# Performance work log

Measured on AMD Instinct MI355X. Metric: run time of the kernel, lower is better.

Reference implementation:

```python
import jax, jax.numpy as jnp
import numpy as np

B, N, D = 4096, 64, 128

def setup_inputs() -> dict:
    key = jax.random.key(0)
    ks = jax.random.split(key, 5)
    return {
        "stu_emb": jax.random.normal(ks[0], (B, D), jnp.float32),
        "concept_emb": jax.random.normal(ks[1], (B, D), jnp.float32),
        "neighbor_emb": jax.random.normal(ks[2], (B, N, D), jnp.float32),
        # Linear(2D -> D) for stu_concept_integration (xavier-like scale)
        "Ws": jax.random.normal(ks[3], (2 * D, D), jnp.float32) * (2.0 / (3 * D)) ** 0.5,
        "bs": jnp.full((D,), 0.1, jnp.float32),
        # Linear(2D -> 1) for concept_neighbor_weight
        "Ww": jax.random.normal(ks[4], (2 * D, 1), jnp.float32) * (2.0 / (2 * D + 1)) ** 0.5,
        "bw": jnp.full((1,), 0.1, jnp.float32),
    }


def reference(stu_emb, concept_emb, neighbor_emb, Ws, bs, Ww, bw):
    # Masks: 1 where the (first) concatenated input is nonzero along features
    dt = stu_emb.dtype
    mask_s = (jnp.sum(stu_emb, -1, keepdims=True) != 0).astype(dt)[:, None, :]      # [B,1,1]
    mask_c = (jnp.sum(concept_emb, -1, keepdims=True) != 0).astype(dt)[:, None, :]  # [B,1,1]

    # Split concat-linear into two halves so the broadcasted half is computed once
    Ws_a, Ws_b = Ws[:D], Ws[D:]   # [D,D] each
    Ww_a, Ww_b = Ww[:D], Ww[D:]   # [D,1] each

    stu_part = stu_emb @ Ws_a            # [B,D]
    con_part = concept_emb @ Ws_b        # [B,D]
    nbr_part = neighbor_emb @ Ws_b       # [B,N,D]

    # neighbor attention weights: Linear(2D->1)(cat(concept_ext, neighbor)) * mask_c
    w = (concept_emb @ Ww_a)[:, None, :] + neighbor_emb @ Ww_b + bw  # [B,N,1]
    w = w * mask_c
    w = jax.nn.softmax(w, axis=-2)  # softmax over neighbor axis

    # stu integrated with neighbors / with the original concept, masked by stu mask
    integ_n = (stu_part[:, None, :] + nbr_part + bs) * mask_s            # [B,N,D]
    integ_o = (stu_part[:, None, :] + con_part[:, None, :] + bs) * mask_s  # [B,N,D] (broadcast)

    # combine over neighbor axis and average the two branches
    y = jnp.sum(integ_o + w * integ_n, axis=-2) / 2  # [B,D]
    return y
```

## Files before the change

### kernel.cpp

```cpp
#include <hip/hip_runtime.h>

#define BB 4096
#define NN 64
#define DD 128
#define G  4
#define P2S 36

#define LDS_BARRIER() asm volatile("s_waitcnt lgkmcnt(0)\n\ts_barrier" ::: "memory")

__global__ __launch_bounds__(256) void kFused(
    const float* __restrict__ stu,
    const float* __restrict__ conc,
    const float* __restrict__ nbr,
    const float* __restrict__ Ws,
    const float* __restrict__ bs,
    const float* __restrict__ Ww,
    float* __restrict__ y)
{
    const int t    = threadIdx.x;
    const int q    = t & 63;
    const int cg   = t & 31;
    const int g8   = t >> 5;
    const int wv   = t >> 6;
    const int b0   = blockIdx.x * G;

    __shared__ __align__(16) float part2[NN * P2S];
    __shared__ float dsum[2][4];
    __shared__ float csum[G];
    __shared__ float maskh[G];
    __shared__ __align__(16) float u[G][2 * DD];
    __shared__ __align__(16) float scratch[G * 8 * DD];

    const float4 wb = reinterpret_cast<const float4*>(Ww + DD)[cg];
    const float4* nb4 = reinterpret_cast<const float4*>(nbr);
    const float4* Ws4 = reinterpret_cast<const float4*>(Ws);

    {
        const int b = b0 + wv;
        float cv0 = conc[(size_t)b * DD + q];
        float cv1 = conc[(size_t)b * DD + 64 + q];
        float sv0 = stu [(size_t)b * DD + q];
        float sv1 = stu [(size_t)b * DD + 64 + q];
        u[wv][q]           = 65.0f * sv0;
        u[wv][64 + q]      = 65.0f * sv1;
        u[wv][DD + q]      = 64.0f * cv0;
        u[wv][DD + 64 + q] = 64.0f * cv1;
        float cs = cv0 + cv1, ss = sv0 + sv1;
#pragma unroll
        for (int o = 1; o < 64; o <<= 1) {
            cs += __shfl_xor(cs, o);
            ss += __shfl_xor(ss, o);
        }
        if (q == 0) {
            csum[wv]  = cs;
            maskh[wv] = (ss != 0.0f) ? 0.5f : 0.0f;
        }
    }

    float4 valA[8], valB[8];
#pragma unroll
    for (int i = 0; i < 8; ++i)
        valA[i] = nb4[(size_t)b0 * 2048 + t + 256 * i];

    const int rown  = 2 * wv + (q & 1) + 8 * ((q >> 1) & 7);
    const int chunk = ((q >> 4) + ((q >> 1) & 7)) & 3;
    const int srcb  = (g8 & 1);

#pragma unroll
    for (int g = 0; g < G; ++g) {
        float4* valc = (g & 1) ? valB : valA;
        float4* valp = (g & 1) ? valA : valB;

#pragma unroll
        for (int i = 0; i < 8; ++i) {
            const int row = g8 + 8 * i;
            part2[row * P2S + cg] =
                valc[i].x * wb.x + valc[i].y * wb.y + valc[i].z * wb.z + valc[i].w * wb.w;
        }
        if (g < G - 1) {
#pragma unroll
            for (int i = 0; i < 8; ++i)
                valp[i] = nb4[(size_t)(b0 + g + 1) * 2048 + t + 256 * i];
        }

        float s;
        {
            const float4 pa = *reinterpret_cast<const float4*>(&part2[rown * P2S + chunk * 8]);
            const float4 pb = *reinterpret_cast<const float4*>(&part2[rown * P2S + chunk * 8 + 4]);
            s = pa.x + pa.y + pa.z + pa.w + pb.x + pb.y + pb.z + pb.w;
            s += __shfl_xor(s, 16);
            s += __shfl_xor(s, 32);
        }
        const float e = __expf(s);
        float s16 = e;
        s16 += __shfl_xor(s16, 1);
        s16 += __shfl_xor(s16, 2);
        s16 += __shfl_xor(s16, 4);
        s16 += __shfl_xor(s16, 8);
        if (q == 0) dsum[g & 1][wv] = s16;
        LDS_BARRIER();

        const float den  = dsum[g & 1][0] + dsum[g & 1][1] + dsum[g & 1][2] + dsum[g & 1][3];
        const float rden = 1.0f / den;
        const bool  uni  = (csum[g] == 0.0f);
        float4 a = {0.f, 0.f, 0.f, 0.f};
#pragma unroll
        for (int i = 0; i < 8; ++i) {
            const float we = __shfl(e, srcb + 2 * i);
            const float w  = uni ? 0.015625f : we * rden;
            a.x += w * valc[i].x; a.y += w * valc[i].y;
            a.z += w * valc[i].z; a.w += w * valc[i].w;
        }
        reinterpret_cast<float4*>(scratch + g * 8 * DD)[g8 * 32 + cg] = a;
    }
    __syncthreads();

#pragma unroll
    for (int it = 0; it < 2; ++it) {
        const int idx = t + 256 * it;
        const int gg  = idx >> 7;
        const int c   = idx & 127;
        float s2 = 0.0f;
#pragma unroll
        for (int k = 0; k < 8; ++k) s2 += scratch[gg * 8 * DD + k * DD + c];
        u[gg][DD + c] += s2;
    }
    __syncthreads();

    float4 acc0 = {0,0,0,0}, acc1 = {0,0,0,0}, acc2 = {0,0,0,0}, acc3 = {0,0,0,0};
#pragma unroll 4
    for (int j = 0; j < 32; ++j) {
        const int k = g8 * 32 + j;
        float4 wq = Ws4[k * 32 + cg];
        float u0 = u[0][k], u1 = u[1][k], u2 = u[2][k], u3 = u[3][k];
        acc0.x += u0 * wq.x; acc0.y += u0 * wq.y; acc0.z += u0 * wq.z; acc0.w += u0 * wq.w;
        acc1.x += u1 * wq.x; acc1.y += u1 * wq.y; acc1.z += u1 * wq.z; acc1.w += u1 * wq.w;
        acc2.x += u2 * wq.x; acc2.y += u2 * wq.y; acc2.z += u2 * wq.z; acc2.w += u2 * wq.w;
        acc3.x += u3 * wq.x; acc3.y += u3 * wq.y; acc3.z += u3 * wq.z; acc3.w += u3 * wq.w;
    }
    {
        float4* pr = reinterpret_cast<float4*>(scratch);
        pr[(g8 * G + 0) * 32 + cg] = acc0;
        pr[(g8 * G + 1) * 32 + cg] = acc1;
        pr[(g8 * G + 2) * 32 + cg] = acc2;
        pr[(g8 * G + 3) * 32 + cg] = acc3;
    }
    __syncthreads();
#pragma unroll
    for (int i = 0; i < 2; ++i) {
        const int idx = t + 256 * i;
        const int r = idx >> 7;
        const int c = idx & 127;
        float s2 = 0.0f;
#pragma unroll
        for (int k2 = 0; k2 < 8; ++k2) s2 += scratch[(k2 * G + r) * DD + c];
        y[(size_t)(b0 + r) * DD + c] = (s2 + 65.0f * bs[c]) * maskh[r];
    }
}

extern "C" void kernel_launch(void* const* d_in, const int* in_sizes, int n_in,
                              void* d_out, int out_size, void* d_ws, size_t ws_size,
                              hipStream_t stream) {
    const float* stu  = (const float*)d_in[0];
    const float* conc = (const float*)d_in[1];
    const float* nbr  = (const float*)d_in[2];
    const float* Ws   = (const float*)d_in[3];
    const float* bs   = (const float*)d_in[4];
    const float* Ww   = (const float*)d_in[5];
    float* y = (float*)d_out;

    kFused<<<BB / G, 256, 0, stream>>>(stu, conc, nbr, Ws, bs, Ww, y);
}
```

Baseline: 29.34 us.

## Restructure fused kernel to 8 batches per 512-thread block with shuffle reductions

Doubles the batch rows per block to 8 and the block size to 512 threads. Each thread now holds two full neighbor rows in registers, so the attention logits come from in-wave shuffle reductions instead of an LDS partial-dot table. The weighted neighbor sum is also reduced with shuffles, and its cross-wave reduction is pipelined into the next batch iteration. The Ws GEMV then processes 8 rows with 4 k-groups, which halves the grid and amortizes Ws loads over more rows, at the cost of fewer blocks and more shuffle traffic.

```diff
diff --git a/kernel.cpp b/kernel.cpp
--- a/kernel.cpp
+++ b/kernel.cpp
@@ -3,12 +3,14 @@
 #define BB 4096
 #define NN 64
 #define DD 128
-#define G  4
-#define P2S 36
+#define G  8
+#define VPS 132
 
 #define LDS_BARRIER() asm volatile("s_waitcnt lgkmcnt(0)\n\ts_barrier" ::: "memory")
 
-__global__ __launch_bounds__(256) void kFused(
+#define DOT4(a, b) ((a).x*(b).x + (a).y*(b).y + (a).z*(b).z + (a).w*(b).w)
+
+__global__ __launch_bounds__(512) void kFused(
     const float* __restrict__ stu,
     const float* __restrict__ conc,
     const float* __restrict__ nbr,
@@ -17,34 +19,42 @@
     const float* __restrict__ Ww,
     float* __restrict__ y)
 {
-    const int t    = threadIdx.x;
-    const int q    = t & 63;
-    const int cg   = t & 31;
-    const int g8   = t >> 5;
-    const int wv   = t >> 6;
-    const int b0   = blockIdx.x * G;
+    const int t  = threadIdx.x;
+    const int q  = t & 63;
+    const int w  = t >> 6;
+    const int b0 = blockIdx.x * G;
 
-    __shared__ __align__(16) float part2[NN * P2S];
-    __shared__ float dsum[2][4];
+    __shared__ __align__(16) float scratch[4096];
+    __shared__ __align__(16) float dsum[2][8];
     __shared__ float csum[G];
     __shared__ float maskh[G];
     __shared__ __align__(16) float u[G][2 * DD];
-    __shared__ __align__(16) float scratch[G * 8 * DD];
 
-    const float4 wb = reinterpret_cast<const float4*>(Ww + DD)[cg];
     const float4* nb4 = reinterpret_cast<const float4*>(nbr);
     const float4* Ws4 = reinterpret_cast<const float4*>(Ws);
+    const float4* Ww4 = reinterpret_cast<const float4*>(Ww + DD);
+    const float4 wb0 = Ww4[2 * (q & 15)];
+    const float4 wb1 = Ww4[2 * (q & 15) + 1];
+
+    float4 vA[4], vB[4];
+    {
+        const size_t tb = (size_t)b0 * 2048;
+        vA[0] = nb4[tb + 2 * t];
+        vA[1] = nb4[tb + 2 * t + 1];
+        vA[2] = nb4[tb + 1024 + 2 * t];
+        vA[3] = nb4[tb + 1024 + 2 * t + 1];
+    }
 
     {
-        const int b = b0 + wv;
+        const int b = b0 + w;
         float cv0 = conc[(size_t)b * DD + q];
         float cv1 = conc[(size_t)b * DD + 64 + q];
         float sv0 = stu [(size_t)b * DD + q];
         float sv1 = stu [(size_t)b * DD + 64 + q];
-        u[wv][q]           = 65.0f * sv0;
-        u[wv][64 + q]      = 65.0f * sv1;
-        u[wv][DD + q]      = 64.0f * cv0;
-        u[wv][DD + 64 + q] = 64.0f * cv1;
+        u[w][q]           = 65.0f * sv0;
+        u[w][64 + q]      = 65.0f * sv1;
+        u[w][DD + q]      = 64.0f * cv0;
+        u[w][DD + 64 + q] = 64.0f * cv1;
         float cs = cv0 + cv1, ss = sv0 + sv1;
 #pragma unroll
         for (int o = 1; o < 64; o <<= 1) {
@@ -52,109 +62,114 @@
             ss += __shfl_xor(ss, o);
         }
         if (q == 0) {
-            csum[wv]  = cs;
-            maskh[wv] = (ss != 0.0f) ? 0.5f : 0.0f;
+            csum[w]  = cs;
+            maskh[w] = (ss != 0.0f) ? 0.5f : 0.0f;
         }
     }
 
-    float4 valA[8], valB[8];
-#pragma unroll
-    for (int i = 0; i < 8; ++i)
-        valA[i] = nb4[(size_t)b0 * 2048 + t + 256 * i];
-
-    const int rown  = 2 * wv + (q & 1) + 8 * ((q >> 1) & 7);
-    const int chunk = ((q >> 4) + ((q >> 1) & 7)) & 3;
-    const int srcb  = (g8 & 1);
-
 #pragma unroll
     for (int g = 0; g < G; ++g) {
-        float4* valc = (g & 1) ? valB : valA;
-        float4* valp = (g & 1) ? valA : valB;
+        float4* valc = (g & 1) ? vB : vA;
+        float4* valp = (g & 1) ? vA : vB;
 
+        float p0 = DOT4(valc[0], wb0) + DOT4(valc[1], wb1);
+        float p1 = DOT4(valc[2], wb0) + DOT4(valc[3], wb1);
 #pragma unroll
-        for (int i = 0; i < 8; ++i) {
-            const int row = g8 + 8 * i;
-            part2[row * P2S + cg] =
-                valc[i].x * wb.x + valc[i].y * wb.y + valc[i].z * wb.z + valc[i].w * wb.w;
+        for (int o = 1; o < 16; o <<= 1) {
+            p0 += __shfl_xor(p0, o);
+            p1 += __shfl_xor(p1, o);
         }
+        const float e0 = __expf(p0);
+        const float e1 = __expf(p1);
+        float es = e0 + e1;
+        es += __shfl_xor(es, 16);
+        es += __shfl_xor(es, 32);
+        if (q == 0) dsum[g & 1][w] = es;
+
         if (g < G - 1) {
-#pragma unroll
-            for (int i = 0; i < 8; ++i)
-                valp[i] = nb4[(size_t)(b0 + g + 1) * 2048 + t + 256 * i];
+            const size_t nb = (size_t)(b0 + g + 1) * 2048;
+            valp[0] = nb4[nb + 2 * t];
+            valp[1] = nb4[nb + 2 * t + 1];
+            valp[2] = nb4[nb + 1024 + 2 * t];
+            valp[3] = nb4[nb + 1024 + 2 * t + 1];
         }
-
-        float s;
-        {
-            const float4 pa = *reinterpret_cast<const float4*>(&part2[rown * P2S + chunk * 8]);
-            const float4 pb = *reinterpret_cast<const float4*>(&part2[rown * P2S + chunk * 8 + 4]);
-            s = pa.x + pa.y + pa.z + pa.w + pb.x + pb.y + pb.z + pb.w;
-            s += __shfl_xor(s, 16);
-            s += __shfl_xor(s, 32);
-        }
-        const float e = __expf(s);
-        float s16 = e;
-        s16 += __shfl_xor(s16, 1);
-        s16 += __shfl_xor(s16, 2);
-        s16 += __shfl_xor(s16, 4);
-        s16 += __shfl_xor(s16, 8);
-        if (q == 0) dsum[g & 1][wv] = s16;
         LDS_BARRIER();
 
-        const float den  = dsum[g & 1][0] + dsum[g & 1][1] + dsum[g & 1][2] + dsum[g & 1][3];
+        const float4 d0 = *reinterpret_cast<const float4*>(&dsum[g & 1][0]);
+        const float4 d1 = *reinterpret_cast<const float4*>(&dsum[g & 1][4]);
+        const float den = d0.x + d0.y + d0.z + d0.w + d1.x + d1.y + d1.z + d1.w;
         const float rden = 1.0f / den;
         const bool  uni  = (csum[g] == 0.0f);
-        float4 a = {0.f, 0.f, 0.f, 0.f};
+        const float w0 = uni ? 0.015625f : e0 * rden;
+        const float w1 = uni ? 0.015625f : e1 * rden;
+        float4 a0, a1;
+        a0.x = w0 * valc[0].x + w1 * valc[2].x;
+        a0.y = w0 * valc[0].y + w1 * valc[2].y;
+        a0.z = w0 * valc[0].z + w1 * valc[2].z;
+        a0.w = w0 * valc[0].w + w1 * valc[2].w;
+        a1.x = w0 * valc[1].x + w1 * valc[3].x;
+        a1.y = w0 * valc[1].y + w1 * valc[3].y;
+        a1.z = w0 * valc[1].z + w1 * valc[3].z;
+        a1.w = w0 * valc[1].w + w1 * valc[3].w;
+        a0.x += __shfl_xor(a0.x, 16); a0.x += __shfl_xor(a0.x, 32);
+        a0.y += __shfl_xor(a0.y, 16); a0.y += __shfl_xor(a0.y, 32);
+        a0.z += __shfl_xor(a0.z, 16); a0.z += __shfl_xor(a0.z, 32);
+        a0.w += __shfl_xor(a0.w, 16); a0.w += __shfl_xor(a0.w, 32);
+        a1.x += __shfl_xor(a1.x, 16); a1.x += __shfl_xor(a1.x, 32);
+        a1.y += __shfl_xor(a1.y, 16); a1.y += __shfl_xor(a1.y, 32);
+        a1.z += __shfl_xor(a1.z, 16); a1.z += __shfl_xor(a1.z, 32);
+        a1.w += __shfl_xor(a1.w, 16); a1.w += __shfl_xor(a1.w, 32);
+        if (q < 16) {
+            float* vp = &scratch[(g & 1) * 2048 + w * VPS + q * 8];
+            *reinterpret_cast<float4*>(vp)     = a0;
+            *reinterpret_cast<float4*>(vp + 4) = a1;
+        }
+        if (g > 0 && t < DD) {
+            const float* vp = &scratch[((g - 1) & 1) * 2048];
+            float s = 0.0f;
 #pragma unroll
-        for (int i = 0; i < 8; ++i) {
-            const float we = __shfl(e, srcb + 2 * i);
-            const float w  = uni ? 0.015625f : we * rden;
-            a.x += w * valc[i].x; a.y += w * valc[i].y;
-            a.z += w * valc[i].z; a.w += w * valc[i].w;
+            for (int k = 0; k < 8; ++k) s += vp[k * VPS + t];
+            u[g - 1][DD + t] += s;
         }
-        reinterpret_cast<float4*>(scratch + g * 8 * DD)[g8 * 32 + cg] = a;
+    }
+
+    LDS_BARRIER();
+    if (t < DD) {
+        const float* vp = &scratch[((G - 1) & 1) * 2048];
+        float s = 0.0f;
+#pragma unroll
+        for (int k = 0; k < 8; ++k) s += vp[k * VPS + t];
+        u[G - 1][DD + t] += s;
     }
     __syncthreads();
 
-#pragma unroll
-    for (int it = 0; it < 2; ++it) {
-        const int idx = t + 256 * it;
-        const int gg  = idx >> 7;
-        const int c   = idx & 127;
-        float s2 = 0.0f;
-#pragma unroll
-        for (int k = 0; k < 8; ++k) s2 += scratch[gg * 8 * DD + k * DD + c];
-        u[gg][DD + c] += s2;
-    }
-    __syncthreads();
-
-    float4 acc0 = {0,0,0,0}, acc1 = {0,0,0,0}, acc2 = {0,0,0,0}, acc3 = {0,0,0,0};
+    const int kg = t >> 7;
+    const int cg = t & 31;
+    const int rh = (t >> 5) & 3;
+    float4 acc0 = {0,0,0,0}, acc1 = {0,0,0,0};
 #pragma unroll 4
-    for (int j = 0; j < 32; ++j) {
-        const int k = g8 * 32 + j;
-        float4 wq = Ws4[k * 32 + cg];
-        float u0 = u[0][k], u1 = u[1][k], u2 = u[2][k], u3 = u[3][k];
+    for (int j = 0; j < 64; ++j) {
+        const int k = kg * 64 + j;
+        const float4 wq = Ws4[k * 32 + cg];
+        const float u0 = u[rh * 2][k], u1 = u[rh * 2 + 1][k];
         acc0.x += u0 * wq.x; acc0.y += u0 * wq.y; acc0.z += u0 * wq.z; acc0.w += u0 * wq.w;
         acc1.x += u1 * wq.x; acc1.y += u1 * wq.y; acc1.z += u1 * wq.z; acc1.w += u1 * wq.w;
-        acc2.x += u2 * wq.x; acc2.y += u2 * wq.y; acc2.z += u2 * wq.z; acc2.w += u2 * wq.w;
-        acc3.x += u3 * wq.x; acc3.y += u3 * wq.y; acc3.z += u3 * wq.z; acc3.w += u3 * wq.w;
     }
     {
         float4* pr = reinterpret_cast<float4*>(scratch);
-        pr[(g8 * G + 0) * 32 + cg] = acc0;
-        pr[(g8 * G + 1) * 32 + cg] = acc1;
-        pr[(g8 * G + 2) * 32 + cg] = acc2;
-        pr[(g8 * G + 3) * 32 + cg] = acc3;
+        pr[(kg * 8 + rh * 2    ) * 32 + cg] = acc0;
+        pr[(kg * 8 + rh * 2 + 1) * 32 + cg] = acc1;
     }
     __syncthreads();
 #pragma unroll
     for (int i = 0; i < 2; ++i) {
-        const int idx = t + 256 * i;
+        const int idx = t + 512 * i;
         const int r = idx >> 7;
         const int c = idx & 127;
-        float s2 = 0.0f;
+        float s = 0.0f;
 #pragma unroll
-        for (int k2 = 0; k2 < 8; ++k2) s2 += scratch[(k2 * G + r) * DD + c];
-        y[(size_t)(b0 + r) * DD + c] = (s2 + 65.0f * bs[c]) * maskh[r];
+        for (int k2 = 0; k2 < 4; ++k2) s += scratch[(k2 * 8 + r) * DD + c];
+        y[(size_t)(b0 + r) * DD + c] = (s + 65.0f * bs[c]) * maskh[r];
     }
 }
 
@@ -169,5 +184,5 @@
     const float* Ww   = (const float*)d_in[5];
     float* y = (float*)d_out;
 
-    kFused<<<BB / G, 256, 0, stream>>>(stu, conc, nbr, Ws, bs, Ww, y);
+    kFused<<<BB / G, 512, 0, stream>>>(stu, conc, nbr, Ws, bs, Ww, y);
 }
```

Result: slower. 33.32 us (+13.6%).

## Split fused kernel into per-batch attention pass and batched GEMV pass

Applied to the files above, without the earlier changes.

Replaces the single fused kernel, where each block handled 4 batch rows with a software-pipelined neighbor loop, with two kernels. The first uses one block per batch row to compute the softmax-weighted neighbor sum and writes it to workspace. The second multiplies 8 rows at a time by Ws, which doubles reuse of each Ws load. This gives more parallelism and less serial work per block in the bandwidth-bound first pass, at the cost of a second launch and a round trip of the intermediate through global memory.

```diff
diff --git a/kernel.cpp b/kernel.cpp
--- a/kernel.cpp
+++ b/kernel.cpp
@@ -3,158 +3,160 @@
 #define BB 4096
 #define NN 64
 #define DD 128
-#define G  4
 #define P2S 36
 
 #define LDS_BARRIER() asm volatile("s_waitcnt lgkmcnt(0)\n\ts_barrier" ::: "memory")
+#define DOT4(a, b) ((a).x*(b).x + (a).y*(b).y + (a).z*(b).z + (a).w*(b).w)
 
-__global__ __launch_bounds__(256) void kFused(
-    const float* __restrict__ stu,
+__global__ __launch_bounds__(256) void k1(
     const float* __restrict__ conc,
     const float* __restrict__ nbr,
-    const float* __restrict__ Ws,
-    const float* __restrict__ bs,
     const float* __restrict__ Ww,
-    float* __restrict__ y)
+    float* __restrict__ vout)
 {
-    const int t    = threadIdx.x;
-    const int q    = t & 63;
-    const int cg   = t & 31;
-    const int g8   = t >> 5;
-    const int wv   = t >> 6;
-    const int b0   = blockIdx.x * G;
+    const int t  = threadIdx.x;
+    const int q  = t & 63;
+    const int cg = t & 31;
+    const int g8 = t >> 5;
+    const int wv = t >> 6;
+    const int b  = blockIdx.x;
 
     __shared__ __align__(16) float part2[NN * P2S];
-    __shared__ float dsum[2][4];
-    __shared__ float csum[G];
-    __shared__ float maskh[G];
-    __shared__ __align__(16) float u[G][2 * DD];
-    __shared__ __align__(16) float scratch[G * 8 * DD];
+    __shared__ float dsum[4];
+    __shared__ __align__(16) float scratch[8 * DD];
 
     const float4 wb = reinterpret_cast<const float4*>(Ww + DD)[cg];
-    const float4* nb4 = reinterpret_cast<const float4*>(nbr);
-    const float4* Ws4 = reinterpret_cast<const float4*>(Ws);
+    const float4* nb4 = reinterpret_cast<const float4*>(nbr) + (size_t)b * 2048;
 
-    {
-        const int b = b0 + wv;
-        float cv0 = conc[(size_t)b * DD + q];
-        float cv1 = conc[(size_t)b * DD + 64 + q];
-        float sv0 = stu [(size_t)b * DD + q];
-        float sv1 = stu [(size_t)b * DD + 64 + q];
-        u[wv][q]           = 65.0f * sv0;
-        u[wv][64 + q]      = 65.0f * sv1;
-        u[wv][DD + q]      = 64.0f * cv0;
-        u[wv][DD + 64 + q] = 64.0f * cv1;
-        float cs = cv0 + cv1, ss = sv0 + sv1;
+    float4 val[8];
 #pragma unroll
-        for (int o = 1; o < 64; o <<= 1) {
-            cs += __shfl_xor(cs, o);
-            ss += __shfl_xor(ss, o);
-        }
-        if (q == 0) {
-            csum[wv]  = cs;
-            maskh[wv] = (ss != 0.0f) ? 0.5f : 0.0f;
-        }
-    }
+    for (int i = 0; i < 8; ++i) val[i] = nb4[t + 256 * i];
 
-    float4 valA[8], valB[8];
+    float cs = conc[(size_t)b * DD + q] + conc[(size_t)b * DD + 64 + q];
+#pragma unroll
+    for (int o = 1; o < 64; o <<= 1) cs += __shfl_xor(cs, o);
+
 #pragma unroll
     for (int i = 0; i < 8; ++i)
-        valA[i] = nb4[(size_t)b0 * 2048 + t + 256 * i];
+        part2[(g8 + 8 * i) * P2S + cg] = DOT4(val[i], wb);
 
     const int rown  = 2 * wv + (q & 1) + 8 * ((q >> 1) & 7);
     const int chunk = ((q >> 4) + ((q >> 1) & 7)) & 3;
-    const int srcb  = (g8 & 1);
+    float s;
+    {
+        const float4 pa = *reinterpret_cast<const float4*>(&part2[rown * P2S + chunk * 8]);
+        const float4 pb = *reinterpret_cast<const float4*>(&part2[rown * P2S + chunk * 8 + 4]);
+        s = pa.x + pa.y + pa.z + pa.w + pb.x + pb.y + pb.z + pb.w;
+        s += __shfl_xor(s, 16);
+        s += __shfl_xor(s, 32);
+    }
+    const float e = __expf(s);
+    float s16 = e;
+    s16 += __shfl_xor(s16, 1);
+    s16 += __shfl_xor(s16, 2);
+    s16 += __shfl_xor(s16, 4);
+    s16 += __shfl_xor(s16, 8);
+    if (q == 0) dsum[wv] = s16;
+    LDS_BARRIER();
+
+    const float rden = 1.0f / (dsum[0] + dsum[1] + dsum[2] + dsum[3]);
+    const bool  uni  = (cs == 0.0f);
+    const int   srcb = g8 & 1;
+    float4 a = {0.f, 0.f, 0.f, 0.f};
+#pragma unroll
+    for (int i = 0; i < 8; ++i) {
+        const float we = __shfl(e, srcb + 2 * i);
+        const float w  = uni ? 0.015625f : we * rden;
+        a.x += w * val[i].x; a.y += w * val[i].y;
+        a.z += w * val[i].z; a.w += w * val[i].w;
+    }
+    reinterpret_cast<float4*>(scratch)[g8 * 32 + cg] = a;
+    __syncthreads();
+
+    if (t < 32) {
+        float4 r = {0.f, 0.f, 0.f, 0.f};
+#pragma unroll
+        for (int k = 0; k < 8; ++k) {
+            const float4 p = reinterpret_cast<const float4*>(scratch)[k * 32 + t];
+            r.x += p.x; r.y += p.y; r.z += p.z; r.w += p.w;
+        }
+        reinterpret_cast<float4*>(vout + (size_t)b * DD)[t] = r;
+    }
+}
+
+__global__ __launch_bounds__(256) void k2(
+    const float* __restrict__ stu,
+    const float* __restrict__ conc,
+    const float* vin,
+    const float* __restrict__ Ws,
+    const float* __restrict__ bs,
+    float* y)
+{
+    const int t  = threadIdx.x;
+    const int q  = t & 63;
+    const int wv = t >> 6;
+    const int cg = t & 31;
+    const int b0 = blockIdx.x * 8;
+
+    __shared__ __align__(16) float u[8][2 * DD];
+    __shared__ __align__(16) float pr[8 * 4 * DD];
+    __shared__ float maskh[8];
 
 #pragma unroll
-    for (int g = 0; g < G; ++g) {
-        float4* valc = (g & 1) ? valB : valA;
-        float4* valp = (g & 1) ? valA : valB;
-
+    for (int rr = wv; rr < 8; rr += 4) {
+        const int b = b0 + rr;
+        const float cv0 = conc[(size_t)b * DD + q];
+        const float cv1 = conc[(size_t)b * DD + 64 + q];
+        const float sv0 = stu [(size_t)b * DD + q];
+        const float sv1 = stu [(size_t)b * DD + 64 + q];
+        const float vv0 = vin [(size_t)b * DD + q];
+        const float vv1 = vin [(size_t)b * DD + 64 + q];
+        u[rr][q]           = 65.0f * sv0;
+        u[rr][64 + q]      = 65.0f * sv1;
+        u[rr][DD + q]      = 64.0f * cv0 + vv0;
+        u[rr][DD + 64 + q] = 64.0f * cv1 + vv1;
+        float ss = sv0 + sv1;
 #pragma unroll
-        for (int i = 0; i < 8; ++i) {
-            const int row = g8 + 8 * i;
-            part2[row * P2S + cg] =
-                valc[i].x * wb.x + valc[i].y * wb.y + valc[i].z * wb.z + valc[i].w * wb.w;
-        }
-        if (g < G - 1) {
-#pragma unroll
-            for (int i = 0; i < 8; ++i)
-                valp[i] = nb4[(size_t)(b0 + g + 1) * 2048 + t + 256 * i];
-        }
-
-        float s;
-        {
-            const float4 pa = *reinterpret_cast<const float4*>(&part2[rown * P2S + chunk * 8]);
-            const float4 pb = *reinterpret_cast<const float4*>(&part2[rown * P2S + chunk * 8 + 4]);
-            s = pa.x + pa.y + pa.z + pa.w + pb.x + pb.y + pb.z + pb.w;
-            s += __shfl_xor(s, 16);
-            s += __shfl_xor(s, 32);
-        }
-        const float e = __expf(s);
-        float s16 = e;
-        s16 += __shfl_xor(s16, 1);
-        s16 += __shfl_xor(s16, 2);
-        s16 += __shfl_xor(s16, 4);
-        s16 += __shfl_xor(s16, 8);
-        if (q == 0) dsum[g & 1][wv] = s16;
-        LDS_BARRIER();
-
-        const float den  = dsum[g & 1][0] + dsum[g & 1][1] + dsum[g & 1][2] + dsum[g & 1][3];
-        const float rden = 1.0f / den;
-        const bool  uni  = (csum[g] == 0.0f);
-        float4 a = {0.f, 0.f, 0.f, 0.f};
-#pragma unroll
-        for (int i = 0; i < 8; ++i) {
-            const float we = __shfl(e, srcb + 2 * i);
-            const float w  = uni ? 0.015625f : we * rden;
-            a.x += w * valc[i].x; a.y += w * valc[i].y;
-            a.z += w * valc[i].z; a.w += w * valc[i].w;
-        }
-        reinterpret_cast<float4*>(scratch + g * 8 * DD)[g8 * 32 + cg] = a;
+        for (int o = 1; o < 64; o <<= 1) ss += __shfl_xor(ss, o);
+        if (q == 0) maskh[rr] = (ss != 0.0f) ? 0.5f : 0.0f;
     }
     __syncthreads();
 
-#pragma unroll
-    for (int it = 0; it < 2; ++it) {
-        const int idx = t + 256 * it;
-        const int gg  = idx >> 7;
-        const int c   = idx & 127;
-        float s2 = 0.0f;
-#pragma unroll
-        for (int k = 0; k < 8; ++k) s2 += scratch[gg * 8 * DD + k * DD + c];
-        u[gg][DD + c] += s2;
-    }
-    __syncthreads();
-
+    const int kg = t >> 6;
+    const int rp = (t >> 5) & 1;
     float4 acc0 = {0,0,0,0}, acc1 = {0,0,0,0}, acc2 = {0,0,0,0}, acc3 = {0,0,0,0};
+    const float4* Ws4 = reinterpret_cast<const float4*>(Ws);
 #pragma unroll 4
-    for (int j = 0; j < 32; ++j) {
-        const int k = g8 * 32 + j;
-        float4 wq = Ws4[k * 32 + cg];
-        float u0 = u[0][k], u1 = u[1][k], u2 = u[2][k], u3 = u[3][k];
+    for (int j = 0; j < 64; ++j) {
+        const int k = kg * 64 + j;
+        const float4 wq = Ws4[k * 32 + cg];
+        const float u0 = u[rp * 4 + 0][k], u1 = u[rp * 4 + 1][k];
+        const float u2 = u[rp * 4 + 2][k], u3 = u[rp * 4 + 3][k];
         acc0.x += u0 * wq.x; acc0.y += u0 * wq.y; acc0.z += u0 * wq.z; acc0.w += u0 * wq.w;
         acc1.x += u1 * wq.x; acc1.y += u1 * wq.y; acc1.z += u1 * wq.z; acc1.w += u1 * wq.w;
         acc2.x += u2 * wq.x; acc2.y += u2 * wq.y; acc2.z += u2 * wq.z; acc2.w += u2 * wq.w;
         acc3.x += u3 * wq.x; acc3.y += u3 * wq.y; acc3.z += u3 * wq.z; acc3.w += u3 * wq.w;
     }
     {
-        float4* pr = reinterpret_cast<float4*>(scratch);
-        pr[(g8 * G + 0) * 32 + cg] = acc0;
-        pr[(g8 * G + 1) * 32 + cg] = acc1;
-        pr[(g8 * G + 2) * 32 + cg] = acc2;
-        pr[(g8 * G + 3) * 32 + cg] = acc3;
+        float4* prr = reinterpret_cast<float4*>(pr);
+        const int gidx = kg * 2 + rp;
+        prr[(gidx * 4 + 0) * 32 + cg] = acc0;
+        prr[(gidx * 4 + 1) * 32 + cg] = acc1;
+        prr[(gidx * 4 + 2) * 32 + cg] = acc2;
+        prr[(gidx * 4 + 3) * 32 + cg] = acc3;
     }
     __syncthreads();
+
 #pragma unroll
-    for (int i = 0; i < 2; ++i) {
+    for (int i = 0; i < 4; ++i) {
         const int idx = t + 256 * i;
         const int r = idx >> 7;
         const int c = idx & 127;
-        float s2 = 0.0f;
+        float s = 0.0f;
 #pragma unroll
-        for (int k2 = 0; k2 < 8; ++k2) s2 += scratch[(k2 * G + r) * DD + c];
-        y[(size_t)(b0 + r) * DD + c] = (s2 + 65.0f * bs[c]) * maskh[r];
+        for (int kk = 0; kk < 4; ++kk)
+            s += pr[((kk * 2 + (r >> 2)) * 4 + (r & 3)) * DD + c];
+        y[(size_t)(b0 + r) * DD + c] = (s + 65.0f * bs[c]) * maskh[r];
     }
 }
 
@@ -169,5 +171,8 @@
     const float* Ww   = (const float*)d_in[5];
     float* y = (float*)d_out;
 
-    kFused<<<BB / G, 256, 0, stream>>>(stu, conc, nbr, Ws, bs, Ww, y);
+    float* v = (ws_size >= (size_t)BB * DD * sizeof(float)) ? (float*)d_ws : y;
+
+    k1<<<BB, 256, 0, stream>>>(conc, nbr, Ww, v);
+    k2<<<BB / 8, 256, 0, stream>>>(stu, conc, v, Ws, bs, y);
 }
```

Result: slower. 33.95 us (+15.7%).
